# Kernel optimization log

Hardware: AMD Instinct MI355X
Metric: run time of the kernel (lower is better)

Reference implementation:

```python
import jax, jax.numpy as jnp
import numpy as np

SIZE = 33
PAD = SIZE // 2
NUM_CLASSES = 19
LOG19 = float(np.log(19.0))
EPS = 1e-6


def _box_sum(x):
    """Depthwise 33x33 all-ones box-sum with zero padding, done separably.
    x: [N, C, H, W] -> [N, C, H, W]
    """
    c = x.shape[1]
    kh = jnp.ones((c, 1, SIZE, 1), x.dtype)
    kw = jnp.ones((c, 1, 1, SIZE), x.dtype)
    dn = ('NCHW', 'OIHW', 'NCHW')
    y = jax.lax.conv_general_dilated(x, kh, (1, 1), [(PAD, PAD), (0, 0)],
                                     dimension_numbers=dn, feature_group_count=c)
    y = jax.lax.conv_general_dilated(y, kw, (1, 1), [(0, 0), (PAD, PAD)],
                                     dimension_numbers=dn, feature_group_count=c)
    return y


def setup_inputs() -> dict:
    key = jax.random.key(0)
    logit = jax.random.normal(key, (1, NUM_CLASSES, 1024, 2048), dtype=jnp.float32)
    return {"logit": logit}


def reference(logit):
    x = logit[0]                                   # [C, H, W]
    p = jax.nn.softmax(x, axis=0)                  # [C, H, W]
    # normalized per-pixel entropy, [1, 1, H, W]
    pixel_entropy = (jnp.sum(-p * jnp.log(p + EPS), axis=0) / LOG19)[None, None]
    region_sum_entropy = _box_sum(pixel_entropy)   # [1, 1, H, W]

    predict = jnp.argmax(p, axis=0)                # [H, W] int
    one_hot = jax.nn.one_hot(predict, NUM_CLASSES, dtype=jnp.float32)  # [H, W, C]
    one_hot = jnp.transpose(one_hot, (2, 0, 1))[None]                  # [1, C, H, W]
    summary = _box_sum(one_hot)                    # per-class region counts
    count = jnp.sum(summary, axis=1, keepdims=True)  # [1, 1, H, W] (= window size)
    dist = summary / count
    region_impurity = jnp.sum(-dist * jnp.log(dist + EPS), axis=1, keepdims=True) / LOG19
    prediction_uncertainty = region_sum_entropy / count
    score = region_impurity * prediction_uncertainty
    return score[0, 0], region_impurity[0, 0], prediction_uncertainty[0, 0]
```

## Files before the change

kernel.cpp:

```cpp
#include <hip/hip_runtime.h>

#define H 1024
#define W 2048
#define HW (H * W)
#define LOG19 2.9444389791664403f
#define TY 4
#define NT 1024
#define GRP 41
#define NGRP 260
#define LGS 9
#define GSS 11

typedef __attribute__((ext_vector_type(4))) float f32x4;
typedef __attribute__((ext_vector_type(2))) float f32x2;

__global__ __launch_bounds__(256) void k1_entropy_argmax(
    const float* __restrict__ logit,
    float* __restrict__ entropy,
    unsigned int* __restrict__ predict4) {
    int q = blockIdx.x * 256 + threadIdx.x;
    int p0 = q * 4;
    f32x4 v[19];
#pragma unroll
    for (int c = 0; c < 19; c++)
        v[c] = *reinterpret_cast<const f32x4*>(logit + (size_t)c * HW + p0);
    f32x4 m = v[0];
    int am[4] = {0, 0, 0, 0};
#pragma unroll
    for (int c = 1; c < 19; c++) {
#pragma unroll
        for (int j = 0; j < 4; j++)
            if (v[c][j] > m[j]) { m[j] = v[c][j]; am[j] = c; }
    }
    f32x4 S = (f32x4)(0.f), T = (f32x4)(0.f);
#pragma unroll
    for (int c = 0; c < 19; c++) {
#pragma unroll
        for (int j = 0; j < 4; j++) {
            float d = v[c][j] - m[j];
            float e = __expf(d);
            S[j] += e;
            T[j] += d * e;
        }
    }
    f32x4 ent;
#pragma unroll
    for (int j = 0; j < 4; j++)
        ent[j] = (__logf(S[j]) - T[j] / S[j]) * (1.0f / LOG19);
    *reinterpret_cast<f32x4*>(entropy + p0) = ent;
    predict4[q] = (unsigned)am[0] | ((unsigned)am[1] << 8) |
                  ((unsigned)am[2] << 16) | ((unsigned)am[3] << 24);
}

#define VACC(yy, SGN)                                                                      \
    {                                                                                      \
        unsigned int pw = *reinterpret_cast<const unsigned short*>(predict + (size_t)(yy)*W + x0); \
        f32x2 ev = *reinterpret_cast<const f32x2*>(entropy + (size_t)(yy)*W + x0);         \
        _Pragma("unroll") for (int j = 0; j < 2; j++) {                                    \
            unsigned int cc = (pw >> (j * 8)) & 0xFFu;                                     \
            unsigned int wi = cc >> 2, bit = 1u << ((cc & 3u) * 8u);                       \
            _Pragma("unroll") for (int k = 0; k < 5; k++)                                  \
                vc[j * 5 + k] SGN## = (wi == (unsigned)k) ? bit : 0u;                      \
            ve[j] SGN## = ev[j];                                                           \
        }                                                                                  \
    }
#define VSLIDE(y)                         \
    {                                     \
        int ya = (y) + 17, yr = (y) - 16; \
        if (ya < H) VACC(ya, +)           \
        if (yr >= 0) VACC(yr, -)          \
    }
#define PUBLISH(b)                                                              \
    {                                                                           \
        unsigned int ps[10];                                                    \
        float pe = ve[0] + ve[1];                                               \
        _Pragma("unroll") for (int k = 0; k < 5; k++) {                         \
            ps[2 * k] = (vc[k] & 0x00FF00FFu) + (vc[5 + k] & 0x00FF00FFu);      \
            ps[2 * k + 1] = ((vc[k] >> 8) & 0x00FF00FFu) +                      \
                            ((vc[5 + k] >> 8) & 0x00FF00FFu);                   \
        }                                                                       \
        _Pragma("unroll") for (int j = 0; j < 2; j++) {                         \
            int i = x0 + 16 + j;                                                \
            int g = i >> 3, sl = i & 7;                                         \
            _Pragma("unroll") for (int k = 0; k < 5; k++)                       \
                lcnt[b][g * GRP + sl * 5 + k] = vc[j * 5 + k];                  \
            lent[b][g * LGS + sl] = ve[j];                                      \
        }                                                                       \
        _Pragma("unroll") for (int q = 0; q < 10; q++) {                        \
            ps[q] += __shfl_xor(ps[q], 1);                                      \
            ps[q] += __shfl_xor(ps[q], 2);                                      \
        }                                                                       \
        pe += __shfl_xor(pe, 1);                                                \
        pe += __shfl_xor(pe, 2);                                                \
        if ((tid & 3) == 0) {                                                   \
            int g = (tid >> 2) + 2;                                             \
            _Pragma("unroll") for (int q = 0; q < 10; q++)                      \
                gsum[b][g * GSS + q] = ps[q];                                   \
            gsum[b][g * GSS + 10] = __float_as_uint(pe);                        \
        }                                                                       \
    }

__global__ __launch_bounds__(NT) void k23_box_score(
    const float* __restrict__ entropy,
    const unsigned char* __restrict__ predict,
    float* __restrict__ out_score,
    float* __restrict__ out_imp,
    float* __restrict__ out_unc) {
    __shared__ float lut[1090];
    __shared__ unsigned int lcnt[2][NGRP * GRP];
    __shared__ float lent[2][NGRP * LGS];
    __shared__ unsigned int gsum[2][NGRP * GSS];
    int tid = threadIdx.x;
    int strip = ((blockIdx.x & 7) << 5) + (blockIdx.x >> 3);
    int y0 = strip * TY;

    for (int n = tid; n < 1090; n += NT)
        lut[n] = n ? (float)n * __logf((float)n) : 0.f;
    if (tid < 64) {
        int b = tid >> 5, t = tid & 31;
        int i = (t < 16) ? t : (2048 + t);
        int g = i >> 3, sl = i & 7;
#pragma unroll
        for (int k = 0; k < 5; k++) lcnt[b][g * GRP + sl * 5 + k] = 0u;
        lent[b][g * LGS + sl] = 0.f;
    }
    if (tid >= 64 && tid < 64 + 88) {
        int idx = tid - 64;
        int b = idx / 44, r = idx % 44;
        int gi = r / 11, q = r % 11;
        int g = (gi < 2) ? gi : (256 + gi);
        gsum[b][g * GSS + q] = 0u;
    }

    int x0 = tid * 2;
    unsigned int vc[10];
#pragma unroll
    for (int i = 0; i < 10; i++) vc[i] = 0u;
    float ve[2] = {0.f, 0.f};
    for (int yy = y0 - 16; yy <= y0 + 16; yy++) {
        if (yy < 0 || yy >= H) continue;
        VACC(yy, +)
    }

#pragma unroll
    for (int p = 0; p < TY / 2; p++) {
        int yA = y0 + 2 * p;
        PUBLISH(0)
        VSLIDE(yA)
        PUBLISH(1)
        if (p < TY / 2 - 1) VSLIDE(yA + 1)
        __syncthreads();

        if (tid < 512) {
            int half = tid >> 8;
            int hq = tid & 255;
            int x0h = hq * 8;
            int y = yA + half;
            unsigned int ha[10];
            float hes;
            {
#pragma unroll
                for (int q = 0; q < 10; q++)
                    ha[q] = gsum[half][hq * GSS + q] + gsum[half][(hq + 1) * GSS + q] +
                            gsum[half][(hq + 2) * GSS + q] + gsum[half][(hq + 3) * GSS + q];
                hes = __uint_as_float(gsum[half][hq * GSS + 10]) +
                      __uint_as_float(gsum[half][(hq + 1) * GSS + 10]) +
                      __uint_as_float(gsum[half][(hq + 2) * GSS + 10]) +
                      __uint_as_float(gsum[half][(hq + 3) * GSS + 10]);
#pragma unroll
                for (int k = 0; k < 5; k++) {
                    unsigned int wv = lcnt[half][(hq + 4) * GRP + k];
                    ha[2 * k] += wv & 0x00FF00FFu;
                    ha[2 * k + 1] += (wv >> 8) & 0x00FF00FFu;
                }
                hes += lent[half][(hq + 4) * LGS];
            }
            int rcount = min(y + 16, H - 1) - max(y - 16, 0) + 1;
            f32x4 osc[2], oim[2], oun[2];
#pragma unroll
            for (int s = 0; s < 8; s++) {
                int x = x0h + s;
                int ccount = min(x + 16, W - 1) - max(x - 16, 0) + 1;
                int Tw = rcount * ccount;
                float invT = 1.0f / (float)Tw;
                float sum = 0.f;
#pragma unroll
                for (int k = 0; k < 5; k++) {
                    unsigned int a = ha[2 * k], b = ha[2 * k + 1];
                    sum += lut[a & 0xFFFFu] + lut[b & 0xFFFFu] + lut[a >> 16];
                    if (k < 4) sum += lut[b >> 16];
                }
                float imp = (lut[Tw] - sum) * invT * (1.0f / LOG19);
                float unc = hes * invT;
                osc[s >> 2][s & 3] = imp * unc;
                oim[s >> 2][s & 3] = imp;
                oun[s >> 2][s & 3] = unc;
                if (s < 7) {
                    int gr = hq, jr = s;
                    int ga = hq + ((s + 33) >> 3), ja = (s + 33) & 7;
                    hes += lent[half][ga * LGS + ja] - lent[half][gr * LGS + jr];
#pragma unroll
                    for (int k = 0; k < 5; k++) {
                        unsigned int wa = lcnt[half][ga * GRP + ja * 5 + k];
                        unsigned int wr = lcnt[half][gr * GRP + jr * 5 + k];
                        ha[2 * k] += (wa & 0x00FF00FFu) - (wr & 0x00FF00FFu);
                        ha[2 * k + 1] += ((wa >> 8) & 0x00FF00FFu) - ((wr >> 8) & 0x00FF00FFu);
                    }
                }
            }
            size_t qo = (size_t)y * W + x0h;
            *reinterpret_cast<f32x4*>(out_score + qo) = osc[0];
            *reinterpret_cast<f32x4*>(out_score + qo + 4) = osc[1];
            *reinterpret_cast<f32x4*>(out_imp + qo) = oim[0];
            *reinterpret_cast<f32x4*>(out_imp + qo + 4) = oim[1];
            *reinterpret_cast<f32x4*>(out_unc + qo) = oun[0];
            *reinterpret_cast<f32x4*>(out_unc + qo + 4) = oun[1];
        }
        __syncthreads();
    }
}

extern "C" void kernel_launch(void* const* d_in, const int* in_sizes, int n_in,
                              void* d_out, int out_size, void* d_ws, size_t ws_size,
                              hipStream_t stream) {
    const float* logit = (const float*)d_in[0];
    float* out = (float*)d_out;
    char* ws = (char*)d_ws;

    float* entropy = (float*)ws;
    unsigned char* predict = (unsigned char*)(ws + (size_t)HW * 4);

    k1_entropy_argmax<<<HW / 1024, 256, 0, stream>>>(logit, entropy, (unsigned int*)predict);
    k23_box_score<<<H / TY, NT, 0, stream>>>(entropy, predict, out, out + HW, out + 2 * HW);
}
```

Measured before the change: 70.19 us.

## Pack fp16 entropy with argmax and split box-score blocks into column halves

```diff
diff --git a/kernel.cpp b/kernel.cpp
--- a/kernel.cpp
+++ b/kernel.cpp
@@ -1,23 +1,40 @@
 #include <hip/hip_runtime.h>
+#include <hip/hip_fp16.h>
 
 #define H 1024
 #define W 2048
 #define HW (H * W)
 #define LOG19 2.9444389791664403f
-#define TY 4
-#define NT 1024
+#define TY 8
+#define NT 576
+#define NVERT 528
+#define BCOLS 1024
+#define PCOLS 1056
+#define NG 132
 #define GRP 41
-#define NGRP 260
 #define LGS 9
 #define GSS 11
 
 typedef __attribute__((ext_vector_type(4))) float f32x4;
-typedef __attribute__((ext_vector_type(2))) float f32x2;
+typedef __attribute__((ext_vector_type(2))) unsigned int u32x2;
+typedef __attribute__((ext_vector_type(4))) unsigned int u32x4;
+
+static __device__ __forceinline__ unsigned short f2h_bits(float f) {
+    __half h = __float2half_rn(f);
+    unsigned short b;
+    __builtin_memcpy(&b, &h, 2);
+    return b;
+}
+static __device__ __forceinline__ float h2f_bits(unsigned int b) {
+    unsigned short s = (unsigned short)b;
+    __half h;
+    __builtin_memcpy(&h, &s, 2);
+    return __half2float(h);
+}
 
 __global__ __launch_bounds__(256) void k1_entropy_argmax(
     const float* __restrict__ logit,
-    float* __restrict__ entropy,
-    unsigned int* __restrict__ predict4) {
+    unsigned int* __restrict__ packed) {
     int q = blockIdx.x * 256 + threadIdx.x;
     int p0 = q * 4;
     f32x4 v[19];
@@ -43,26 +60,26 @@
             T[j] += d * e;
         }
     }
-    f32x4 ent;
-#pragma unroll
-    for (int j = 0; j < 4; j++)
-        ent[j] = (__logf(S[j]) - T[j] / S[j]) * (1.0f / LOG19);
-    *reinterpret_cast<f32x4*>(entropy + p0) = ent;
-    predict4[q] = (unsigned)am[0] | ((unsigned)am[1] << 8) |
-                  ((unsigned)am[2] << 16) | ((unsigned)am[3] << 24);
-}
-
-#define VACC(yy, SGN)                                                                      \
-    {                                                                                      \
-        unsigned int pw = *reinterpret_cast<const unsigned short*>(predict + (size_t)(yy)*W + x0); \
-        f32x2 ev = *reinterpret_cast<const f32x2*>(entropy + (size_t)(yy)*W + x0);         \
-        _Pragma("unroll") for (int j = 0; j < 2; j++) {                                    \
-            unsigned int cc = (pw >> (j * 8)) & 0xFFu;                                     \
-            unsigned int wi = cc >> 2, bit = 1u << ((cc & 3u) * 8u);                       \
-            _Pragma("unroll") for (int k = 0; k < 5; k++)                                  \
-                vc[j * 5 + k] SGN## = (wi == (unsigned)k) ? bit : 0u;                      \
-            ve[j] SGN## = ev[j];                                                           \
-        }                                                                                  \
+    u32x4 w;
+#pragma unroll
+    for (int j = 0; j < 4; j++) {
+        float ent = (__logf(S[j]) - T[j] / S[j]) * (1.0f / LOG19);
+        w[j] = (unsigned int)f2h_bits(ent) | ((unsigned int)am[j] << 24);
+    }
+    *reinterpret_cast<u32x4*>(packed + p0) = w;
+}
+
+#define VACC(yy, SGN)                                                                   \
+    if (vvalid) {                                                                       \
+        u32x2 pw = *reinterpret_cast<const u32x2*>(packed + (size_t)(yy)*W + gcol0);    \
+        _Pragma("unroll") for (int j = 0; j < 2; j++) {                                 \
+            unsigned int wv = pw[j];                                                    \
+            unsigned int cc = wv >> 24;                                                 \
+            unsigned int wi = cc >> 2, bit = 1u << ((cc & 3u) * 8u);                    \
+            _Pragma("unroll") for (int k = 0; k < 5; k++)                               \
+                vc[j * 5 + k] SGN## = (wi == (unsigned)k) ? bit : 0u;                   \
+            ve[j] SGN## = h2f_bits(wv);                                                 \
+        }                                                                               \
     }
 #define VSLIDE(y)                         \
     {                                     \
@@ -71,7 +88,7 @@
         if (yr >= 0) VACC(yr, -)          \
     }
 #define PUBLISH(b)                                                              \
-    {                                                                           \
+    if (tid < NVERT) {                                                          \
         unsigned int ps[10];                                                    \
         float pe = ve[0] + ve[1];                                               \
         _Pragma("unroll") for (int k = 0; k < 5; k++) {                         \
@@ -79,13 +96,13 @@
             ps[2 * k + 1] = ((vc[k] >> 8) & 0x00FF00FFu) +                      \
                             ((vc[5 + k] >> 8) & 0x00FF00FFu);                   \
         }                                                                       \
-        _Pragma("unroll") for (int j = 0; j < 2; j++) {                         \
-            int i = x0 + 16 + j;                                                \
-            int g = i >> 3, sl = i & 7;                                         \
-            _Pragma("unroll") for (int k = 0; k < 5; k++)                       \
-                lcnt[b][g * GRP + sl * 5 + k] = vc[j * 5 + k];                  \
-            lent[b][g * LGS + sl] = ve[j];                                      \
-        }                                                                       \
+        int g = tid >> 2, sl0 = (2 * tid) & 7;                                  \
+        _Pragma("unroll") for (int k = 0; k < 5; k++) {                         \
+            lcnt[b][g * GRP + sl0 * 5 + k] = vc[k];                             \
+            lcnt[b][g * GRP + (sl0 + 1) * 5 + k] = vc[5 + k];                   \
+        }                                                                       \
+        lent[b][g * LGS + sl0] = ve[0];                                         \
+        lent[b][g * LGS + sl0 + 1] = ve[1];                                     \
         _Pragma("unroll") for (int q = 0; q < 10; q++) {                        \
             ps[q] += __shfl_xor(ps[q], 1);                                      \
             ps[q] += __shfl_xor(ps[q], 2);                                      \
@@ -93,7 +110,6 @@
         pe += __shfl_xor(pe, 1);                                                \
         pe += __shfl_xor(pe, 2);                                                \
         if ((tid & 3) == 0) {                                                   \
-            int g = (tid >> 2) + 2;                                             \
             _Pragma("unroll") for (int q = 0; q < 10; q++)                      \
                 gsum[b][g * GSS + q] = ps[q];                                   \
             gsum[b][g * GSS + 10] = __float_as_uint(pe);                        \
@@ -101,45 +117,33 @@
     }
 
 __global__ __launch_bounds__(NT) void k23_box_score(
-    const float* __restrict__ entropy,
-    const unsigned char* __restrict__ predict,
+    const unsigned int* __restrict__ packed,
     float* __restrict__ out_score,
     float* __restrict__ out_imp,
     float* __restrict__ out_unc) {
     __shared__ float lut[1090];
-    __shared__ unsigned int lcnt[2][NGRP * GRP];
-    __shared__ float lent[2][NGRP * LGS];
-    __shared__ unsigned int gsum[2][NGRP * GSS];
+    __shared__ unsigned int lcnt[2][NG * GRP];
+    __shared__ float lent[2][NG * LGS];
+    __shared__ unsigned int gsum[2][NG * GSS];
     int tid = threadIdx.x;
-    int strip = ((blockIdx.x & 7) << 5) + (blockIdx.x >> 3);
+    int bid = blockIdx.x;
+    int xcd = bid & 7, idx = bid >> 3;
+    int strip = xcd * 16 + (idx >> 1);
+    int colbase = (idx & 1) * BCOLS;
     int y0 = strip * TY;
 
     for (int n = tid; n < 1090; n += NT)
         lut[n] = n ? (float)n * __logf((float)n) : 0.f;
-    if (tid < 64) {
-        int b = tid >> 5, t = tid & 31;
-        int i = (t < 16) ? t : (2048 + t);
-        int g = i >> 3, sl = i & 7;
-#pragma unroll
-        for (int k = 0; k < 5; k++) lcnt[b][g * GRP + sl * 5 + k] = 0u;
-        lent[b][g * LGS + sl] = 0.f;
-    }
-    if (tid >= 64 && tid < 64 + 88) {
-        int idx = tid - 64;
-        int b = idx / 44, r = idx % 44;
-        int gi = r / 11, q = r % 11;
-        int g = (gi < 2) ? gi : (256 + gi);
-        gsum[b][g * GSS + q] = 0u;
-    }
-
-    int x0 = tid * 2;
+
+    int gcol0 = colbase - 16 + 2 * tid;
+    bool vvalid = (tid < NVERT) && ((unsigned)gcol0 < (unsigned)W);
     unsigned int vc[10];
 #pragma unroll
     for (int i = 0; i < 10; i++) vc[i] = 0u;
     float ve[2] = {0.f, 0.f};
-    for (int yy = y0 - 16; yy <= y0 + 16; yy++) {
-        if (yy < 0 || yy >= H) continue;
-        VACC(yy, +)
+    {
+        int ylo = max(y0 - 16, 0), yhi = min(y0 + 16, H - 1);
+        for (int yy = ylo; yy <= yhi; yy++) VACC(yy, +)
     }
 
 #pragma unroll
@@ -148,39 +152,38 @@
         PUBLISH(0)
         VSLIDE(yA)
         PUBLISH(1)
-        if (p < TY / 2 - 1) VSLIDE(yA + 1)
         __syncthreads();
 
-        if (tid < 512) {
-            int half = tid >> 8;
-            int hq = tid & 255;
+        if (tid < 256) {
+            int rsel = tid >> 7;
+            int hq = tid & 127;
             int x0h = hq * 8;
-            int y = yA + half;
+            int y = yA + rsel;
             unsigned int ha[10];
             float hes;
             {
 #pragma unroll
                 for (int q = 0; q < 10; q++)
-                    ha[q] = gsum[half][hq * GSS + q] + gsum[half][(hq + 1) * GSS + q] +
-                            gsum[half][(hq + 2) * GSS + q] + gsum[half][(hq + 3) * GSS + q];
-                hes = __uint_as_float(gsum[half][hq * GSS + 10]) +
-                      __uint_as_float(gsum[half][(hq + 1) * GSS + 10]) +
-                      __uint_as_float(gsum[half][(hq + 2) * GSS + 10]) +
-                      __uint_as_float(gsum[half][(hq + 3) * GSS + 10]);
+                    ha[q] = gsum[rsel][hq * GSS + q] + gsum[rsel][(hq + 1) * GSS + q] +
+                            gsum[rsel][(hq + 2) * GSS + q] + gsum[rsel][(hq + 3) * GSS + q];
+                hes = __uint_as_float(gsum[rsel][hq * GSS + 10]) +
+                      __uint_as_float(gsum[rsel][(hq + 1) * GSS + 10]) +
+                      __uint_as_float(gsum[rsel][(hq + 2) * GSS + 10]) +
+                      __uint_as_float(gsum[rsel][(hq + 3) * GSS + 10]);
 #pragma unroll
                 for (int k = 0; k < 5; k++) {
-                    unsigned int wv = lcnt[half][(hq + 4) * GRP + k];
+                    unsigned int wv = lcnt[rsel][(hq + 4) * GRP + k];
                     ha[2 * k] += wv & 0x00FF00FFu;
                     ha[2 * k + 1] += (wv >> 8) & 0x00FF00FFu;
                 }
-                hes += lent[half][(hq + 4) * LGS];
+                hes += lent[rsel][(hq + 4) * LGS];
             }
             int rcount = min(y + 16, H - 1) - max(y - 16, 0) + 1;
             f32x4 osc[2], oim[2], oun[2];
 #pragma unroll
             for (int s = 0; s < 8; s++) {
-                int x = x0h + s;
-                int ccount = min(x + 16, W - 1) - max(x - 16, 0) + 1;
+                int gx = colbase + x0h + s;
+                int ccount = min(gx + 16, W - 1) - max(gx - 16, 0) + 1;
                 int Tw = rcount * ccount;
                 float invT = 1.0f / (float)Tw;
                 float sum = 0.f;
@@ -196,19 +199,18 @@
                 oim[s >> 2][s & 3] = imp;
                 oun[s >> 2][s & 3] = unc;
                 if (s < 7) {
-                    int gr = hq, jr = s;
                     int ga = hq + ((s + 33) >> 3), ja = (s + 33) & 7;
-                    hes += lent[half][ga * LGS + ja] - lent[half][gr * LGS + jr];
+                    hes += lent[rsel][ga * LGS + ja] - lent[rsel][hq * LGS + s];
 #pragma unroll
                     for (int k = 0; k < 5; k++) {
-                        unsigned int wa = lcnt[half][ga * GRP + ja * 5 + k];
-                        unsigned int wr = lcnt[half][gr * GRP + jr * 5 + k];
+                        unsigned int wa = lcnt[rsel][ga * GRP + ja * 5 + k];
+                        unsigned int wr = lcnt[rsel][hq * GRP + s * 5 + k];
                         ha[2 * k] += (wa & 0x00FF00FFu) - (wr & 0x00FF00FFu);
                         ha[2 * k + 1] += ((wa >> 8) & 0x00FF00FFu) - ((wr >> 8) & 0x00FF00FFu);
                     }
                 }
             }
-            size_t qo = (size_t)y * W + x0h;
+            size_t qo = (size_t)y * W + colbase + x0h;
             *reinterpret_cast<f32x4*>(out_score + qo) = osc[0];
             *reinterpret_cast<f32x4*>(out_score + qo + 4) = osc[1];
             *reinterpret_cast<f32x4*>(out_imp + qo) = oim[0];
@@ -216,6 +218,7 @@
             *reinterpret_cast<f32x4*>(out_unc + qo) = oun[0];
             *reinterpret_cast<f32x4*>(out_unc + qo + 4) = oun[1];
         }
+        if (p < TY / 2 - 1) VSLIDE(yA + 1)
         __syncthreads();
     }
 }
@@ -225,11 +228,8 @@
                               hipStream_t stream) {
     const float* logit = (const float*)d_in[0];
     float* out = (float*)d_out;
-    char* ws = (char*)d_ws;
-
-    float* entropy = (float*)ws;
-    unsigned char* predict = (unsigned char*)(ws + (size_t)HW * 4);
-
-    k1_entropy_argmax<<<HW / 1024, 256, 0, stream>>>(logit, entropy, (unsigned int*)predict);
-    k23_box_score<<<H / TY, NT, 0, stream>>>(entropy, predict, out, out + HW, out + 2 * HW);
-}
+    unsigned int* packed = (unsigned int*)d_ws;
+
+    k1_entropy_argmax<<<HW / 1024, 256, 0, stream>>>(logit, packed);
+    k23_box_score<<<256, NT, 0, stream>>>(packed, out, out + HW, out + 2 * HW);
+}
```

Measured after the change: 72.53 us. 3.3% more time.
